# Performance work log

Hardware: AMD Instinct MI355X
Metric: run time of the kernel (lower is better)

Reference implementation:

```python
import jax, jax.numpy as jnp
import numpy as np

B, T, D = 4, 2048, 1024
H = 16
HD = D // H          # per-head dim (dk/heads = dv/heads = 64)
FF = 2048            # FFN default hidden_dim
EPS = 1e-5


def _ln(x, g, b):
    mu = jnp.mean(x, -1, keepdims=True)
    var = jnp.mean((x - mu) ** 2, -1, keepdims=True)
    return (x - mu) * jax.lax.rsqrt(var + EPS) * g + b


def setup_inputs() -> dict:
    key = jax.random.key(0)
    ks = jax.random.split(key, 12)
    s_in = 1.0 / np.sqrt(D)
    s_ff = 1.0 / np.sqrt(FF)
    return {
        "x": jax.random.normal(ks[0], (B, T, D), jnp.float32),
        # per-head projections stacked: [H, D, HD]
        "Wq": jax.random.uniform(ks[1], (H, D, HD), jnp.float32, -s_in, s_in),
        "bq": jnp.zeros((H, HD), jnp.float32),
        "Wk": jax.random.uniform(ks[2], (H, D, HD), jnp.float32, -s_in, s_in),
        "bk": jnp.zeros((H, HD), jnp.float32),
        "Wv": jax.random.uniform(ks[3], (H, D, HD), jnp.float32, -s_in, s_in),
        "bv": jnp.zeros((H, HD), jnp.float32),
        "Wo": jax.random.uniform(ks[4], (D, D), jnp.float32, -s_in, s_in),
        "bo": jnp.zeros((D,), jnp.float32),
        "ln1_g": jnp.ones((D,), jnp.float32),
        "ln1_b": jnp.zeros((D,), jnp.float32),
        "W1": jax.random.uniform(ks[5], (D, FF), jnp.float32, -s_in, s_in),
        "b1": jnp.zeros((FF,), jnp.float32),
        "W2": jax.random.uniform(ks[6], (FF, D), jnp.float32, -s_ff, s_ff),
        "b2": jnp.zeros((D,), jnp.float32),
        "ln2_g": jnp.ones((D,), jnp.float32),
        "ln2_b": jnp.zeros((D,), jnp.float32),
    }


def reference(x, Wq, bq, Wk, bk, Wv, bv, Wo, bo, ln1_g, ln1_b, W1, b1, W2, b2, ln2_g, ln2_b):
    # QKV projections (per-head Linear loop vectorized over H): [B,H,T,HD]
    q = jnp.einsum("btd,hdk->bhtk", x, Wq) + bq[:, None, :]
    k = jnp.einsum("btd,hdk->bhtk", x, Wk) + bk[:, None, :]
    v = jnp.einsum("btd,hdk->bhtk", x, Wv) + bv[:, None, :]
    # scaled dot-product attention; scale uses per-head dk = HD
    scores = jnp.einsum("bhtk,bhsk->bhts", q, k) / jnp.sqrt(jnp.float32(HD))
    weights = jax.nn.softmax(scores, axis=-1)
    ctx = jnp.einsum("bhts,bhsk->bhtk", weights, v)        # [B,H,T,HD]
    # concat heads along last dim (head order preserved) then output proj
    ctx = ctx.transpose(0, 2, 1, 3).reshape(B, T, D)
    c = ctx @ Wo + bo
    # residual + LayerNorm
    x = _ln(x + c, ln1_g, ln1_b)
    # FFN: Linear -> ReLU -> Linear
    y = jax.nn.relu(x @ W1 + b1) @ W2 + b2
    return _ln(x + y, ln2_g, ln2_b)
```

## Files before the change

### kernel.cpp

```cpp
#include <hip/hip_runtime.h>
#include <hip/hip_bf16.h>

#define BB 4
#define TT 2048
#define DD 1024
#define HH 16
#define HD 64
#define FF 2048
#define QSCL 0.1803368801111204f

typedef unsigned short u16;
typedef __bf16 bf16x8 __attribute__((ext_vector_type(8)));
typedef float f32x4 __attribute__((ext_vector_type(4)));
typedef float f32x16 __attribute__((ext_vector_type(16)));
typedef unsigned short u16x8 __attribute__((ext_vector_type(8)));
typedef unsigned short u16x4 __attribute__((ext_vector_type(4)));
typedef unsigned int u32x4 __attribute__((ext_vector_type(4)));

__device__ __forceinline__ u16 f2bf(float f) {
    return __builtin_bit_cast(u16, (__bf16)f);
}
__device__ __forceinline__ float bf2f(u16 u) {
    return __builtin_bit_cast(float, (unsigned)u << 16);
}
__device__ __forceinline__ float exp2fast(float x) {
    float r;
    asm("v_exp_f32 %0, %1" : "=v"(r) : "v"(x));
    return r;
}
__device__ __forceinline__ void gload16(const void* g, void* l) {
    __builtin_amdgcn_global_load_lds((const __attribute__((address_space(1))) void*)g,
                                     (__attribute__((address_space(3))) void*)l, 16, 0, 0);
}

__global__ __launch_bounds__(256) void convert_x(const float* __restrict__ in, u16* __restrict__ out, int n8) {
    int i = blockIdx.x * 256 + threadIdx.x;
    if (i >= n8) return;
    const float4* p = (const float4*)in + (size_t)i * 2;
    float4 a = p[0], b = p[1];
    u16x8 o;
    o[0] = f2bf(a.x); o[1] = f2bf(a.y); o[2] = f2bf(a.z); o[3] = f2bf(a.w);
    o[4] = f2bf(b.x); o[5] = f2bf(b.y); o[6] = f2bf(b.z); o[7] = f2bf(b.w);
    ((u16x8*)out)[i] = o;
}

__global__ __launch_bounds__(256) void transpose_conv(const float* __restrict__ in, u16* __restrict__ out, int R, int C) {
    __shared__ float tile[32][33];
    const int c0 = blockIdx.x * 32, r0 = blockIdx.y * 32;
    const int tx = threadIdx.x & 31, ty = threadIdx.x >> 5;
#pragma unroll
    for (int j = 0; j < 4; ++j) tile[ty + j * 8][tx] = in[(size_t)(r0 + ty + j * 8) * C + c0 + tx];
    __syncthreads();
#pragma unroll
    for (int j = 0; j < 4; ++j) out[(size_t)(c0 + ty + j * 8) * R + r0 + tx] = f2bf(tile[tx][ty + j * 8]);
}

__global__ __launch_bounds__(256) void qkv_transpose(const float* __restrict__ Wq, const float* __restrict__ Wk,
                                                     const float* __restrict__ Wv, u16* __restrict__ out) {
    __shared__ float tile[32][33];
    const int z = blockIdx.z, w = z >> 4, h = z & 15;
    const float* in = (w == 0 ? Wq : (w == 1 ? Wk : Wv)) + (size_t)h * (DD * HD);
    u16* op = out + (size_t)(w * 1024 + h * 64) * DD;
    const int c0 = blockIdx.x * 32, r0 = blockIdx.y * 32;
    const int tx = threadIdx.x & 31, ty = threadIdx.x >> 5;
#pragma unroll
    for (int j = 0; j < 4; ++j) tile[ty + j * 8][tx] = in[(size_t)(r0 + ty + j * 8) * HD + c0 + tx];
    __syncthreads();
#pragma unroll
    for (int j = 0; j < 4; ++j) op[(size_t)(c0 + ty + j * 8) * DD + r0 + tx] = f2bf(tile[tx][ty + j * 8]);
}

__global__ __launch_bounds__(256) void pack_bias(const float* __restrict__ bq, const float* __restrict__ bk,
                                                 const float* __restrict__ bv, float* __restrict__ out) {
    int i = blockIdx.x * 256 + threadIdx.x;
    if (i < 3072) {
        const float* s = i < 1024 ? bq : (i < 2048 ? bk : bv);
        out[i] = s[i & 1023];
    }
}

#define GBM 128
#define GBN 128
#define GBK 64

template <int EPI>
__global__ __launch_bounds__(256) void gemm_bt(const u16* __restrict__ A, const u16* __restrict__ Bt,
                                               const float* __restrict__ bias, const void* __restrict__ res,
                                               void* __restrict__ outp, void* __restrict__ outp2,
                                               int M, int N, int K) {
    __shared__ __align__(16) u16 sA[GBM * GBK];
    __shared__ __align__(16) u16 sB[GBN * GBK];
    const int t = threadIdx.x;
    const int lane = t & 63, wv = t >> 6;
    const int wm = (wv >> 1) * 64, wn = (wv & 1) * 64;
    const int lq = lane & 15, lk8 = (lane >> 4) * 8;
    const int nwg = gridDim.x * gridDim.y;
    const int bid = blockIdx.y * gridDim.x + blockIdx.x;
    const int swz = (bid & 7) * (nwg >> 3) + (bid >> 3);
    const int m0 = (swz / gridDim.x) * GBM, n0 = (swz % gridDim.x) * GBN;

    const int lr = lane >> 3, ch = lane & 7;
    const int colel = (ch ^ lr) << 3;
    const u16* Abase = A + (size_t)(m0 + wv * 32 + lr) * K + colel;
    const u16* Bbase = Bt + (size_t)(n0 + wv * 32 + lr) * K + colel;
    char* sAw = (char*)sA + wv * 32 * 128;
    char* sBw = (char*)sB + wv * 32 * 128;

    f32x4 acc[4][4];
#pragma unroll
    for (int i = 0; i < 4; ++i)
#pragma unroll
        for (int j = 0; j < 4; ++j) acc[i][j] = (f32x4){0.f, 0.f, 0.f, 0.f};

    for (int k0 = 0; k0 < K; k0 += GBK) {
#pragma unroll
        for (int i = 0; i < 4; ++i) {
            gload16(Abase + (size_t)i * 8 * K + k0, sAw + i * 1024);
            gload16(Bbase + (size_t)i * 8 * K + k0, sBw + i * 1024);
        }
        __syncthreads();
#pragma unroll
        for (int kk = 0; kk < 2; ++kk) {
            bf16x8 af[4], bfr[4];
#pragma unroll
            for (int mf = 0; mf < 4; ++mf) {
                int row = wm + mf * 16 + lq;
                int by = (row * 128 + kk * 64 + lk8 * 2) ^ ((row & 7) << 4);
                af[mf] = *(const bf16x8*)((const char*)sA + by);
            }
#pragma unroll
            for (int nf = 0; nf < 4; ++nf) {
                int row = wn + nf * 16 + lq;
                int by = (row * 128 + kk * 64 + lk8 * 2) ^ ((row & 7) << 4);
                bfr[nf] = *(const bf16x8*)((const char*)sB + by);
            }
#pragma unroll
            for (int mf = 0; mf < 4; ++mf)
#pragma unroll
                for (int nf = 0; nf < 4; ++nf)
                    acc[mf][nf] = __builtin_amdgcn_mfma_f32_16x16x32_bf16(af[mf], bfr[nf], acc[mf][nf], 0, 0, 0);
        }
        __syncthreads();
    }

    const int rbase = (lane >> 4) * 4;
#pragma unroll
    for (int mf = 0; mf < 4; ++mf) {
#pragma unroll
        for (int nf = 0; nf < 4; ++nf) {
            int gn = n0 + wn + nf * 16 + lq;
            float bv = bias[gn];
#pragma unroll
            for (int r = 0; r < 4; ++r) {
                int gm = m0 + wm + mf * 16 + rbase + r;
                size_t idx = (size_t)gm * N + gn;
                float val = acc[mf][nf][r] + bv;
                if (EPI == 2) {
                    ((u16*)outp)[idx] = f2bf(val > 0.f ? val : 0.f);
                } else if (EPI == 1) {
                    ((u16*)outp)[idx] = f2bf(val + ((const float*)res)[idx]);
                } else {
                    ((u16*)outp)[idx] = f2bf(val + bf2f(((const u16*)res)[idx]));
                }
            }
        }
    }
}

template <int EPI>
__global__ __launch_bounds__(512, 2) void gemm256(const u16* __restrict__ A, const u16* __restrict__ Bt,
                                                  const float* __restrict__ bias,
                                                  void* __restrict__ outp, void* __restrict__ outp2,
                                                  int M, int N, int K) {
    __shared__ __align__(16) u16 sA[2][256 * 64];
    __shared__ __align__(16) u16 sB[2][256 * 64];
    const int t = threadIdx.x;
    const int lane = t & 63, wv = t >> 6;
    const int wm = (wv >> 2) * 128, wn = (wv & 3) * 64;
    const int lq = lane & 15, lk8 = (lane >> 4) * 8;
    const int lr = lane >> 3, ch = lane & 7;
    const int colel = (ch ^ lr) << 3;
    const int nwg = gridDim.x * gridDim.y;
    const int bid = blockIdx.y * gridDim.x + blockIdx.x;
    const int swz = (bid & 7) * (nwg >> 3) + (bid >> 3);
    const int m0 = (swz / gridDim.x) * 256, n0 = (swz % gridDim.x) * 256;

    const u16* Ag = A + ((size_t)m0 + lr) * K + colel;
    const u16* Bg = Bt + ((size_t)n0 + lr) * K + colel;

#define STAGE_A(buf, slot, k0)                                                        \
    do {                                                                              \
        _Pragma("unroll") for (int j = 0; j < 2; ++j) {                               \
            int row0 = (slot)*64 + j * 128 + wv * 8;                                  \
            gload16(Ag + (size_t)row0 * K + (k0), (char*)sA + (buf)*32768 + row0 * 128); \
        }                                                                             \
    } while (0)
#define STAGE_B(buf, slot, k0)                                                        \
    do {                                                                              \
        _Pragma("unroll") for (int j = 0; j < 2; ++j) {                               \
            int c = j * 8 + wv;                                                       \
            int row0 = (c >> 2) * 64 + (slot)*32 + (c & 3) * 8;                       \
            gload16(Bg + (size_t)row0 * K + (k0), (char*)sB + (buf)*32768 + row0 * 128); \
        }                                                                             \
    } while (0)

    f32x4 acc[8][4];
#pragma unroll
    for (int i = 0; i < 8; ++i)
#pragma unroll
        for (int j = 0; j < 4; ++j) acc[i][j] = (f32x4){0.f, 0.f, 0.f, 0.f};

    STAGE_A(0, 0, 0);
    STAGE_B(0, 0, 0);
    STAGE_B(0, 1, 0);
    STAGE_A(0, 1, 0);
    asm volatile("s_waitcnt vmcnt(0)" ::: "memory");
    __builtin_amdgcn_s_barrier();
    __builtin_amdgcn_sched_barrier(0);

    const int nk = K / 64;
    for (int kt = 0; kt < nk; ++kt) {
        const int cur = kt & 1, nxt = cur ^ 1;
        const int k1 = (kt + 1) * 64;
        const bool pf = (kt + 1 < nk);
        const char* sAc = (const char*)sA + cur * 32768;
        const char* sBc = (const char*)sB + cur * 32768;
        bf16x8 a[4][2], b[4][2];

#pragma unroll
        for (int mf = 0; mf < 4; ++mf)
#pragma unroll
            for (int kk = 0; kk < 2; ++kk) {
                int row = wm + mf * 16 + lq;
                a[mf][kk] = *(const bf16x8*)(sAc + ((row * 128 + kk * 64 + lk8 * 2) ^ ((row & 7) << 4)));
            }
#pragma unroll
        for (int nf = 0; nf < 4; ++nf)
#pragma unroll
            for (int kk = 0; kk < 2; ++kk) {
                int row = wn + nf * 16 + lq;
                b[nf][kk] = *(const bf16x8*)(sBc + ((row * 128 + kk * 64 + lk8 * 2) ^ ((row & 7) << 4)));
            }
        if (pf) {
            STAGE_A(nxt, 0, k1);
            STAGE_B(nxt, 0, k1);
            STAGE_B(nxt, 1, k1);
        }
        asm volatile("s_waitcnt lgkmcnt(0)" ::: "memory");
        __builtin_amdgcn_sched_barrier(0);
        __builtin_amdgcn_s_setprio(1);
#pragma unroll
        for (int mf = 0; mf < 4; ++mf)
#pragma unroll
            for (int nf = 0; nf < 4; ++nf) {
                acc[mf][nf] = __builtin_amdgcn_mfma_f32_16x16x32_bf16(a[mf][0], b[nf][0], acc[mf][nf], 0, 0, 0);
                acc[mf][nf] = __builtin_amdgcn_mfma_f32_16x16x32_bf16(a[mf][1], b[nf][1], acc[mf][nf], 0, 0, 0);
            }
        __builtin_amdgcn_s_setprio(0);
        __builtin_amdgcn_sched_barrier(0);
        if (pf)
            asm volatile("s_waitcnt vmcnt(6)" ::: "memory");
        else
            asm volatile("s_waitcnt vmcnt(0)" ::: "memory");
        __builtin_amdgcn_s_barrier();
        __builtin_amdgcn_sched_barrier(0);

#pragma unroll
        for (int mf = 0; mf < 4; ++mf)
#pragma unroll
            for (int kk = 0; kk < 2; ++kk) {
                int row = wm + 64 + mf * 16 + lq;
                a[mf][kk] = *(const bf16x8*)(sAc + ((row * 128 + kk * 64 + lk8 * 2) ^ ((row & 7) << 4)));
            }
        if (pf) STAGE_A(nxt, 1, k1);
        asm volatile("s_waitcnt lgkmcnt(0)" ::: "memory");
        __builtin_amdgcn_sched_barrier(0);
        __builtin_amdgcn_s_setprio(1);
#pragma unroll
        for (int mf = 0; mf < 4; ++mf)
#pragma unroll
            for (int nf = 0; nf < 4; ++nf) {
                acc[mf + 4][nf] = __builtin_amdgcn_mfma_f32_16x16x32_bf16(a[mf][0], b[nf][0], acc[mf + 4][nf], 0, 0, 0);
                acc[mf + 4][nf] = __builtin_amdgcn_mfma_f32_16x16x32_bf16(a[mf][1], b[nf][1], acc[mf + 4][nf], 0, 0, 0);
            }
        __builtin_amdgcn_s_setprio(0);
        __builtin_amdgcn_sched_barrier(0);
        if (pf)
            asm volatile("s_waitcnt vmcnt(2)" ::: "memory");
        __builtin_amdgcn_s_barrier();
        __builtin_amdgcn_sched_barrier(0);
    }

    const int rbase = (lane >> 4) * 4;
#pragma unroll
    for (int mf = 0; mf < 8; ++mf) {
#pragma unroll
        for (int nf = 0; nf < 4; ++nf) {
            int gn = n0 + wn + nf * 16 + lq;
            float bv = bias[gn];
            if (EPI == 0) {
                int which = gn >> 10, hh = (gn >> 6) & 15, hd = gn & 63;
                int gm0 = m0 + wm + mf * 16 + rbase;
                int b2 = gm0 >> 11, tt2 = gm0 & 2047;
                if (which == 2) {
                    u16x4 pk;
#pragma unroll
                    for (int r = 0; r < 4; ++r) pk[r] = f2bf(acc[mf][nf][r] + bv);
                    *(u16x4*)((u16*)outp2 + ((size_t)(b2 * HH + hh) * HD + hd) * TT + tt2) = pk;
                } else {
                    float scl = (which == 0) ? QSCL : 1.f;
                    size_t off0 = (size_t)which * ((size_t)BB * HH * TT * HD) +
                                  ((size_t)(b2 * HH + hh) * TT + tt2) * HD + hd;
#pragma unroll
                    for (int r = 0; r < 4; ++r)
                        ((u16*)outp)[off0 + (size_t)r * HD] = f2bf((acc[mf][nf][r] + bv) * scl);
                }
            } else {
#pragma unroll
                for (int r = 0; r < 4; ++r) {
                    int gm = m0 + wm + mf * 16 + rbase + r;
                    float val = acc[mf][nf][r] + bv;
                    ((u16*)outp)[(size_t)gm * N + gn] = f2bf(val > 0.f ? val : 0.f);
                }
            }
        }
    }
#undef STAGE_A
#undef STAGE_B
}

__global__ __launch_bounds__(512) void attn_kernel(const u16* __restrict__ qk, const u16* __restrict__ vt,
                                                   u16* __restrict__ ctx) {
    const int t = threadIdx.x, wv = t >> 6, lane = t & 63;
    const int l31 = lane & 31, hi = lane >> 5;
    const int lr = lane >> 3, ch = lane & 7;
    const int colel = (ch ^ lr) << 3;
    const int bid = blockIdx.y * 8 + blockIdx.x;
    const int swz = (bid & 7) * 64 + (bid >> 3);
    const int qt = swz & 7, bh = swz >> 3;
    const size_t WSTR = (size_t)BB * HH * TT * HD;
    const u16* qp = qk + (size_t)bh * TT * HD;
    const u16* kp = qp + WSTR;
    const u16* vtp = vt + (size_t)bh * HD * TT;
    const int qr = qt * 256 + wv * 32;

    __shared__ __align__(16) u16 sK[2][64 * 64];
    __shared__ __align__(16) u16 sVt[2][64 * 64];

    const u16* kbase = kp + (size_t)(wv * 8 + lr) * HD + colel;
    const u16* vbase = vtp + (size_t)(wv * 8 + lr) * TT + colel;
    char* dK = (char*)sK + wv * 1024;
    char* dV = (char*)sVt + wv * 1024;

#define ATTN_STAGE(bufi, kb)                                        \
    do {                                                            \
        gload16(kbase + (size_t)(kb)*HD, dK + (bufi)*8192);         \
        gload16(vbase + (kb), dV + (bufi)*8192);                    \
    } while (0)

    bf16x8 qf[4];
#pragma unroll
    for (int c = 0; c < 4; ++c)
        qf[c] = *(const bf16x8*)(qp + (size_t)(qr + l31) * HD + c * 16 + 8 * hi);

    int off[2][4];
#pragma unroll
    for (int half = 0; half < 2; ++half)
#pragma unroll
        for (int c = 0; c < 4; ++c) {
            int row = half * 32 + l31;
            off[half][c] = row * 128 + (((c * 16 + 8 * hi) * 2) ^ ((row & 7) << 4));
        }

    f32x16 psv = (f32x16)0.f;
    f32x16 oacc[2];
    oacc[0] = (f32x16)0.f;
    oacc[1] = (f32x16)0.f;

    ATTN_STAGE(0, 0);

    const int NT = TT / 64;
    for (int kt = 0; kt < NT; ++kt) {
        const int cur = kt & 1;
        if (kt + 1 < NT) {
            ATTN_STAGE(cur ^ 1, (kt + 1) * 64);
            asm volatile("s_waitcnt vmcnt(2)" ::: "memory");
        } else {
            asm volatile("s_waitcnt vmcnt(0)" ::: "memory");
        }
        __builtin_amdgcn_s_barrier();
        __builtin_amdgcn_sched_barrier(0);

        const char* sKc = (const char*)sK + cur * 8192;
        const char* sVc = (const char*)sVt + cur * 8192;

        f32x16 sacc[2];
        sacc[0] = (f32x16)0.f;
        sacc[1] = (f32x16)0.f;
#pragma unroll
        for (int kb2 = 0; kb2 < 2; ++kb2)
#pragma unroll
            for (int c = 0; c < 4; ++c) {
                bf16x8 kf = *(const bf16x8*)(sKc + off[kb2][c]);
                sacc[kb2] = __builtin_amdgcn_mfma_f32_32x32x16_bf16(kf, qf[c], sacc[kb2], 0, 0, 0);
            }

#pragma unroll
        for (int kb2 = 0; kb2 < 2; ++kb2) {
#pragma unroll
            for (int i = 0; i < 16; ++i) sacc[kb2][i] = exp2fast(sacc[kb2][i]);
            psv += sacc[kb2];
        }

        bf16x8 pfrag[4];
#pragma unroll
        for (int kb2 = 0; kb2 < 2; ++kb2)
#pragma unroll
            for (int c2 = 0; c2 < 2; ++c2) {
                const int base = c2 * 8;
                unsigned a0, a1, b0, b1;
                asm("v_cvt_pk_bf16_f32 %0, %1, %2" : "=v"(a0) : "v"(sacc[kb2][base + 0]), "v"(sacc[kb2][base + 1]));
                asm("v_cvt_pk_bf16_f32 %0, %1, %2" : "=v"(a1) : "v"(sacc[kb2][base + 2]), "v"(sacc[kb2][base + 3]));
                asm("v_cvt_pk_bf16_f32 %0, %1, %2" : "=v"(b0) : "v"(sacc[kb2][base + 4]), "v"(sacc[kb2][base + 5]));
                asm("v_cvt_pk_bf16_f32 %0, %1, %2" : "=v"(b1) : "v"(sacc[kb2][base + 6]), "v"(sacc[kb2][base + 7]));
                asm("v_permlane32_swap_b32 %0, %1" : "+v"(a0), "+v"(b0));
                asm("v_permlane32_swap_b32 %0, %1" : "+v"(a1), "+v"(b1));
                u32x4 w = {a0, a1, b0, b1};
                pfrag[kb2 * 2 + c2] = __builtin_bit_cast(bf16x8, w);
            }

#pragma unroll
        for (int db = 0; db < 2; ++db)
#pragma unroll
            for (int kc = 0; kc < 4; ++kc) {
                bf16x8 vf = *(const bf16x8*)(sVc + off[db][kc]);
                oacc[db] = __builtin_amdgcn_mfma_f32_32x32x16_bf16(vf, pfrag[kc], oacc[db], 0, 0, 0);
            }

        __builtin_amdgcn_sched_barrier(0);
        __builtin_amdgcn_s_barrier();
    }

    float ls = 0.f;
#pragma unroll
    for (int i = 0; i < 16; ++i) ls += psv[i];
    ls += __shfl_xor(ls, 32);
    const float inv = 1.f / ls;

    const int b = bh >> 4, h = bh & 15;
    u16* orow = ctx + ((size_t)b * TT + (qr + l31)) * DD + h * HD;
#pragma unroll
    for (int db = 0; db < 2; ++db)
#pragma unroll
        for (int rq = 0; rq < 4; ++rq) {
            u16x4 ov;
#pragma unroll
            for (int j = 0; j < 4; ++j) ov[j] = f2bf(oacc[db][rq * 4 + j] * inv);
            *(u16x4*)(orow + db * 32 + rq * 8 + 4 * hi) = ov;
        }
#undef ATTN_STAGE
}

template <bool OUTF32>
__global__ __launch_bounds__(256) void ln_kernel(const u16* __restrict__ y, const float* __restrict__ g,
                                                 const float* __restrict__ b, float* __restrict__ of,
                                                 u16* __restrict__ ob) {
    const int row = blockIdx.x, t = threadIdx.x;
    const u16x4 raw = *(const u16x4*)(y + (size_t)row * DD + t * 4);
    float v0 = bf2f(raw[0]), v1 = bf2f(raw[1]), v2 = bf2f(raw[2]), v3 = bf2f(raw[3]);
    float s = v0 + v1 + v2 + v3;
    float q = v0 * v0 + v1 * v1 + v2 * v2 + v3 * v3;
#pragma unroll
    for (int m = 1; m < 64; m <<= 1) {
        s += __shfl_xor(s, m);
        q += __shfl_xor(q, m);
    }
    __shared__ float red[8];
    const int wv = t >> 6, ln = t & 63;
    if (ln == 0) {
        red[wv] = s;
        red[4 + wv] = q;
    }
    __syncthreads();
    s = red[0] + red[1] + red[2] + red[3];
    q = red[4] + red[5] + red[6] + red[7];
    const float mu = s * (1.f / DD);
    const float var = q * (1.f / DD) - mu * mu;
    const float rstd = rsqrtf(var + 1e-5f);
    const float4 gg = ((const float4*)g)[t];
    const float4 bb = ((const float4*)b)[t];
    float o0 = (v0 - mu) * rstd * gg.x + bb.x;
    float o1 = (v1 - mu) * rstd * gg.y + bb.y;
    float o2 = (v2 - mu) * rstd * gg.z + bb.z;
    float o3 = (v3 - mu) * rstd * gg.w + bb.w;
    if (OUTF32) {
        ((float4*)(of + (size_t)row * DD))[t] = (float4){o0, o1, o2, o3};
    } else {
        u16x4 u;
        u[0] = f2bf(o0); u[1] = f2bf(o1); u[2] = f2bf(o2); u[3] = f2bf(o3);
        *(u16x4*)(ob + (size_t)row * DD + t * 4) = u;
    }
}

extern "C" void kernel_launch(void* const* d_in, const int* in_sizes, int n_in,
                              void* d_out, int out_size, void* d_ws, size_t ws_size,
                              hipStream_t stream) {
    const float* x   = (const float*)d_in[0];
    const float* Wq  = (const float*)d_in[1];
    const float* bq  = (const float*)d_in[2];
    const float* Wk  = (const float*)d_in[3];
    const float* bk  = (const float*)d_in[4];
    const float* Wv  = (const float*)d_in[5];
    const float* bv  = (const float*)d_in[6];
    const float* Wo  = (const float*)d_in[7];
    const float* bo  = (const float*)d_in[8];
    const float* g1  = (const float*)d_in[9];
    const float* be1 = (const float*)d_in[10];
    const float* W1  = (const float*)d_in[11];
    const float* b1  = (const float*)d_in[12];
    const float* W2  = (const float*)d_in[13];
    const float* b2  = (const float*)d_in[14];
    const float* g2  = (const float*)d_in[15];
    const float* be2 = (const float*)d_in[16];
    float* out = (float*)d_out;

    char* ws = (char*)d_ws;
    u16*   xb    = (u16*)(ws + 0);
    u16*   wqkvt = (u16*)(ws + 16777216);
    u16*   wot   = (u16*)(ws + 23068672);
    u16*   w1t   = (u16*)(ws + 25165824);
    u16*   w2t   = (u16*)(ws + 29360128);
    float* bqkv  = (float*)(ws + 33554432);
    u16*   qkb   = (u16*)(ws + 33566720);
    u16*   vtb   = qkb + (size_t)2 * BB * HH * TT * HD;
    u16*   y1b   = (u16*)(ws + 83898368);
    u16*   x1b   = (u16*)(ws + 100675584);
    u16*   ctx   = xb;
    u16*   hbuf  = qkb;
    u16*   y2b   = y1b;

    const int M = BB * TT;

    convert_x<<<dim3((M * DD / 8 + 255) / 256), 256, 0, stream>>>(x, xb, M * DD / 8);
    qkv_transpose<<<dim3(2, 32, 48), 256, 0, stream>>>(Wq, Wk, Wv, wqkvt);
    transpose_conv<<<dim3(32, 32), 256, 0, stream>>>(Wo, wot, DD, DD);
    transpose_conv<<<dim3(64, 32), 256, 0, stream>>>(W1, w1t, DD, FF);
    transpose_conv<<<dim3(32, 64), 256, 0, stream>>>(W2, w2t, FF, DD);
    pack_bias<<<dim3(12), 256, 0, stream>>>(bq, bk, bv, bqkv);

    gemm256<0><<<dim3(3 * DD / 256, M / 256), 512, 0, stream>>>(xb, wqkvt, bqkv, qkb, vtb, M, 3 * DD, DD);
    attn_kernel<<<dim3(TT / 256, BB * HH), 512, 0, stream>>>(qkb, vtb, ctx);
    gemm_bt<1><<<dim3(DD / GBN, M / GBM), 256, 0, stream>>>(ctx, wot, bo, x, y1b, nullptr, M, DD, DD);
    ln_kernel<false><<<dim3(M), 256, 0, stream>>>(y1b, g1, be1, nullptr, x1b);
    gemm256<2><<<dim3(FF / 256, M / 256), 512, 0, stream>>>(x1b, w1t, b1, hbuf, nullptr, M, FF, DD);
    gemm_bt<3><<<dim3(DD / GBN, M / GBM), 256, 0, stream>>>(hbuf, w2t, b2, x1b, y2b, nullptr, M, DD, FF);
    ln_kernel<true><<<dim3(M), 256, 0, stream>>>(y2b, g2, be2, out, nullptr);
}
```

Before: 289.7 us.

## Process 64 query rows per wave in attention with 256-thread blocks

```diff
diff --git a/kernel.cpp b/kernel.cpp
--- a/kernel.cpp
+++ b/kernel.cpp
@@ -329,7 +329,7 @@
 #undef STAGE_B
 }
 
-__global__ __launch_bounds__(512) void attn_kernel(const u16* __restrict__ qk, const u16* __restrict__ vt,
+__global__ __launch_bounds__(256) void attn_kernel(const u16* __restrict__ qk, const u16* __restrict__ vt,
                                                    u16* __restrict__ ctx) {
     const int t = threadIdx.x, wv = t >> 6, lane = t & 63;
     const int l31 = lane & 31, hi = lane >> 5;
@@ -342,26 +342,30 @@
     const u16* qp = qk + (size_t)bh * TT * HD;
     const u16* kp = qp + WSTR;
     const u16* vtp = vt + (size_t)bh * HD * TT;
-    const int qr = qt * 256 + wv * 32;
+    const int qr = qt * 256 + wv * 64;
 
     __shared__ __align__(16) u16 sK[2][64 * 64];
     __shared__ __align__(16) u16 sVt[2][64 * 64];
 
-    const u16* kbase = kp + (size_t)(wv * 8 + lr) * HD + colel;
-    const u16* vbase = vtp + (size_t)(wv * 8 + lr) * TT + colel;
-    char* dK = (char*)sK + wv * 1024;
-    char* dV = (char*)sVt + wv * 1024;
-
-#define ATTN_STAGE(bufi, kb)                                        \
-    do {                                                            \
-        gload16(kbase + (size_t)(kb)*HD, dK + (bufi)*8192);         \
-        gload16(vbase + (kb), dV + (bufi)*8192);                    \
+    const u16* kbase = kp + (size_t)(wv * 16 + lr) * HD + colel;
+    const u16* vbase = vtp + (size_t)(wv * 16 + lr) * TT + colel;
+    char* dK = (char*)sK + wv * 16 * 128;
+    char* dV = (char*)sVt + wv * 16 * 128;
+
+#define ATTN_STAGE(bufi, kb)                                                              \
+    do {                                                                                  \
+        _Pragma("unroll") for (int ii = 0; ii < 2; ++ii) {                                \
+            gload16(kbase + (size_t)((kb) + ii * 8) * HD, dK + (bufi)*8192 + ii * 1024);  \
+            gload16(vbase + (size_t)(ii * 8) * TT + (kb), dV + (bufi)*8192 + ii * 1024);  \
+        }                                                                                 \
     } while (0)
 
-    bf16x8 qf[4];
-#pragma unroll
-    for (int c = 0; c < 4; ++c)
-        qf[c] = *(const bf16x8*)(qp + (size_t)(qr + l31) * HD + c * 16 + 8 * hi);
+    bf16x8 qf[2][4];
+#pragma unroll
+    for (int qg = 0; qg < 2; ++qg)
+#pragma unroll
+        for (int c = 0; c < 4; ++c)
+            qf[qg][c] = *(const bf16x8*)(qp + (size_t)(qr + qg * 32 + l31) * HD + c * 16 + 8 * hi);
 
     int off[2][4];
 #pragma unroll
@@ -372,10 +376,13 @@
             off[half][c] = row * 128 + (((c * 16 + 8 * hi) * 2) ^ ((row & 7) << 4));
         }
 
-    f32x16 psv = (f32x16)0.f;
-    f32x16 oacc[2];
-    oacc[0] = (f32x16)0.f;
-    oacc[1] = (f32x16)0.f;
+    float ls[2] = {0.f, 0.f};
+    f32x16 oacc[2][2];
+#pragma unroll
+    for (int qg = 0; qg < 2; ++qg) {
+        oacc[qg][0] = (f32x16)0.f;
+        oacc[qg][1] = (f32x16)0.f;
+    }
 
     ATTN_STAGE(0, 0);
 
@@ -384,7 +391,7 @@
         const int cur = kt & 1;
         if (kt + 1 < NT) {
             ATTN_STAGE(cur ^ 1, (kt + 1) * 64);
-            asm volatile("s_waitcnt vmcnt(2)" ::: "memory");
+            asm volatile("s_waitcnt vmcnt(4)" ::: "memory");
         } else {
             asm volatile("s_waitcnt vmcnt(0)" ::: "memory");
         }
@@ -394,70 +401,78 @@
         const char* sKc = (const char*)sK + cur * 8192;
         const char* sVc = (const char*)sVt + cur * 8192;
 
-        f32x16 sacc[2];
-        sacc[0] = (f32x16)0.f;
-        sacc[1] = (f32x16)0.f;
+        f32x16 sacc[2][2];
+#pragma unroll
+        for (int qg = 0; qg < 2; ++qg) {
+            sacc[qg][0] = (f32x16)0.f;
+            sacc[qg][1] = (f32x16)0.f;
+        }
 #pragma unroll
         for (int kb2 = 0; kb2 < 2; ++kb2)
 #pragma unroll
             for (int c = 0; c < 4; ++c) {
                 bf16x8 kf = *(const bf16x8*)(sKc + off[kb2][c]);
-                sacc[kb2] = __builtin_amdgcn_mfma_f32_32x32x16_bf16(kf, qf[c], sacc[kb2], 0, 0, 0);
-            }
-
-#pragma unroll
-        for (int kb2 = 0; kb2 < 2; ++kb2) {
-#pragma unroll
-            for (int i = 0; i < 16; ++i) sacc[kb2][i] = exp2fast(sacc[kb2][i]);
-            psv += sacc[kb2];
-        }
-
-        bf16x8 pfrag[4];
-#pragma unroll
-        for (int kb2 = 0; kb2 < 2; ++kb2)
-#pragma unroll
-            for (int c2 = 0; c2 < 2; ++c2) {
-                const int base = c2 * 8;
-                unsigned a0, a1, b0, b1;
-                asm("v_cvt_pk_bf16_f32 %0, %1, %2" : "=v"(a0) : "v"(sacc[kb2][base + 0]), "v"(sacc[kb2][base + 1]));
-                asm("v_cvt_pk_bf16_f32 %0, %1, %2" : "=v"(a1) : "v"(sacc[kb2][base + 2]), "v"(sacc[kb2][base + 3]));
-                asm("v_cvt_pk_bf16_f32 %0, %1, %2" : "=v"(b0) : "v"(sacc[kb2][base + 4]), "v"(sacc[kb2][base + 5]));
-                asm("v_cvt_pk_bf16_f32 %0, %1, %2" : "=v"(b1) : "v"(sacc[kb2][base + 6]), "v"(sacc[kb2][base + 7]));
-                asm("v_permlane32_swap_b32 %0, %1" : "+v"(a0), "+v"(b0));
-                asm("v_permlane32_swap_b32 %0, %1" : "+v"(a1), "+v"(b1));
-                u32x4 w = {a0, a1, b0, b1};
-                pfrag[kb2 * 2 + c2] = __builtin_bit_cast(bf16x8, w);
-            }
+                sacc[0][kb2] = __builtin_amdgcn_mfma_f32_32x32x16_bf16(kf, qf[0][c], sacc[0][kb2], 0, 0, 0);
+                sacc[1][kb2] = __builtin_amdgcn_mfma_f32_32x32x16_bf16(kf, qf[1][c], sacc[1][kb2], 0, 0, 0);
+            }
+
+        bf16x8 pfrag[2][4];
+#pragma unroll
+        for (int qg = 0; qg < 2; ++qg) {
+#pragma unroll
+            for (int kb2 = 0; kb2 < 2; ++kb2)
+#pragma unroll
+                for (int i = 0; i < 16; ++i) sacc[qg][kb2][i] = exp2fast(sacc[qg][kb2][i]);
+            f32x16 sm = sacc[qg][0] + sacc[qg][1];
+            float s8 = ((sm[0] + sm[1]) + (sm[2] + sm[3])) + ((sm[4] + sm[5]) + (sm[6] + sm[7]));
+            float s16 = ((sm[8] + sm[9]) + (sm[10] + sm[11])) + ((sm[12] + sm[13]) + (sm[14] + sm[15]));
+            ls[qg] += s8 + s16;
+#pragma unroll
+            for (int kb2 = 0; kb2 < 2; ++kb2)
+#pragma unroll
+                for (int c2 = 0; c2 < 2; ++c2) {
+                    const int base = c2 * 8;
+                    unsigned a0, a1, b0, b1;
+                    asm("v_cvt_pk_bf16_f32 %0, %1, %2" : "=v"(a0) : "v"(sacc[qg][kb2][base + 0]), "v"(sacc[qg][kb2][base + 1]));
+                    asm("v_cvt_pk_bf16_f32 %0, %1, %2" : "=v"(a1) : "v"(sacc[qg][kb2][base + 2]), "v"(sacc[qg][kb2][base + 3]));
+                    asm("v_cvt_pk_bf16_f32 %0, %1, %2" : "=v"(b0) : "v"(sacc[qg][kb2][base + 4]), "v"(sacc[qg][kb2][base + 5]));
+                    asm("v_cvt_pk_bf16_f32 %0, %1, %2" : "=v"(b1) : "v"(sacc[qg][kb2][base + 6]), "v"(sacc[qg][kb2][base + 7]));
+                    asm("v_permlane32_swap_b32 %0, %1" : "+v"(a0), "+v"(b0));
+                    asm("v_permlane32_swap_b32 %0, %1" : "+v"(a1), "+v"(b1));
+                    u32x4 w = {a0, a1, b0, b1};
+                    pfrag[qg][kb2 * 2 + c2] = __builtin_bit_cast(bf16x8, w);
+                }
+        }
 
 #pragma unroll
         for (int db = 0; db < 2; ++db)
 #pragma unroll
             for (int kc = 0; kc < 4; ++kc) {
                 bf16x8 vf = *(const bf16x8*)(sVc + off[db][kc]);
-                oacc[db] = __builtin_amdgcn_mfma_f32_32x32x16_bf16(vf, pfrag[kc], oacc[db], 0, 0, 0);
+                oacc[0][db] = __builtin_amdgcn_mfma_f32_32x32x16_bf16(vf, pfrag[0][kc], oacc[0][db], 0, 0, 0);
+                oacc[1][db] = __builtin_amdgcn_mfma_f32_32x32x16_bf16(vf, pfrag[1][kc], oacc[1][db], 0, 0, 0);
             }
 
         __builtin_amdgcn_sched_barrier(0);
         __builtin_amdgcn_s_barrier();
     }
 
-    float ls = 0.f;
-#pragma unroll
-    for (int i = 0; i < 16; ++i) ls += psv[i];
-    ls += __shfl_xor(ls, 32);
-    const float inv = 1.f / ls;
-
     const int b = bh >> 4, h = bh & 15;
-    u16* orow = ctx + ((size_t)b * TT + (qr + l31)) * DD + h * HD;
-#pragma unroll
-    for (int db = 0; db < 2; ++db)
-#pragma unroll
-        for (int rq = 0; rq < 4; ++rq) {
-            u16x4 ov;
-#pragma unroll
-            for (int j = 0; j < 4; ++j) ov[j] = f2bf(oacc[db][rq * 4 + j] * inv);
-            *(u16x4*)(orow + db * 32 + rq * 8 + 4 * hi) = ov;
-        }
+#pragma unroll
+    for (int qg = 0; qg < 2; ++qg) {
+        float l2 = ls[qg] + __shfl_xor(ls[qg], 32);
+        const float inv = 1.f / l2;
+        u16* orow = ctx + ((size_t)b * TT + (qr + qg * 32 + l31)) * DD + h * HD;
+#pragma unroll
+        for (int db = 0; db < 2; ++db)
+#pragma unroll
+            for (int rq = 0; rq < 4; ++rq) {
+                u16x4 ov;
+#pragma unroll
+                for (int j = 0; j < 4; ++j) ov[j] = f2bf(oacc[qg][db][rq * 4 + j] * inv);
+                *(u16x4*)(orow + db * 32 + rq * 8 + 4 * hi) = ov;
+            }
+    }
 #undef ATTN_STAGE
 }
 
@@ -549,7 +564,7 @@
     pack_bias<<<dim3(12), 256, 0, stream>>>(bq, bk, bv, bqkv);
 
     gemm256<0><<<dim3(3 * DD / 256, M / 256), 512, 0, stream>>>(xb, wqkvt, bqkv, qkb, vtb, M, 3 * DD, DD);
-    attn_kernel<<<dim3(TT / 256, BB * HH), 512, 0, stream>>>(qkb, vtb, ctx);
+    attn_kernel<<<dim3(8, BB * HH), 256, 0, stream>>>(qkb, vtb, ctx);
     gemm_bt<1><<<dim3(DD / GBN, M / GBM), 256, 0, stream>>>(ctx, wot, bo, x, y1b, nullptr, M, DD, DD);
     ln_kernel<false><<<dim3(M), 256, 0, stream>>>(y1b, g1, be1, nullptr, x1b);
     gemm256<2><<<dim3(FF / 256, M / 256), 512, 0, stream>>>(x1b, w1t, b1, hbuf, nullptr, M, FF, DD);
```

Result: slower. 324.5 us (+12.0%).

## Route Wo and W2 GEMMs through double-buffered gemm256 with 256x128 tiles

Applied to the files above, without the earlier changes.

```diff
diff --git a/kernel.cpp b/kernel.cpp
--- a/kernel.cpp
+++ b/kernel.cpp
@@ -79,140 +79,52 @@
     }
 }
 
-#define GBM 128
-#define GBN 128
-#define GBK 64
-
-template <int EPI>
-__global__ __launch_bounds__(256) void gemm_bt(const u16* __restrict__ A, const u16* __restrict__ Bt,
-                                               const float* __restrict__ bias, const void* __restrict__ res,
-                                               void* __restrict__ outp, void* __restrict__ outp2,
-                                               int M, int N, int K) {
-    __shared__ __align__(16) u16 sA[GBM * GBK];
-    __shared__ __align__(16) u16 sB[GBN * GBK];
+template <int EPI, int BN>
+__global__ __launch_bounds__(512, 2) void gemm256(const u16* __restrict__ A, const u16* __restrict__ Bt,
+                                                  const float* __restrict__ bias, const void* __restrict__ res,
+                                                  void* __restrict__ outp, void* __restrict__ outp2,
+                                                  int M, int N, int K) {
+    constexpr int NFR = BN / 64;
+    constexpr int NB = BN / 64;
+    __shared__ __align__(16) u16 sA[2][256 * 64];
+    __shared__ __align__(16) u16 sB[2][BN * 64];
     const int t = threadIdx.x;
     const int lane = t & 63, wv = t >> 6;
-    const int wm = (wv >> 1) * 64, wn = (wv & 1) * 64;
-    const int lq = lane & 15, lk8 = (lane >> 4) * 8;
-    const int nwg = gridDim.x * gridDim.y;
-    const int bid = blockIdx.y * gridDim.x + blockIdx.x;
-    const int swz = (bid & 7) * (nwg >> 3) + (bid >> 3);
-    const int m0 = (swz / gridDim.x) * GBM, n0 = (swz % gridDim.x) * GBN;
-
-    const int lr = lane >> 3, ch = lane & 7;
-    const int colel = (ch ^ lr) << 3;
-    const u16* Abase = A + (size_t)(m0 + wv * 32 + lr) * K + colel;
-    const u16* Bbase = Bt + (size_t)(n0 + wv * 32 + lr) * K + colel;
-    char* sAw = (char*)sA + wv * 32 * 128;
-    char* sBw = (char*)sB + wv * 32 * 128;
-
-    f32x4 acc[4][4];
-#pragma unroll
-    for (int i = 0; i < 4; ++i)
-#pragma unroll
-        for (int j = 0; j < 4; ++j) acc[i][j] = (f32x4){0.f, 0.f, 0.f, 0.f};
-
-    for (int k0 = 0; k0 < K; k0 += GBK) {
-#pragma unroll
-        for (int i = 0; i < 4; ++i) {
-            gload16(Abase + (size_t)i * 8 * K + k0, sAw + i * 1024);
-            gload16(Bbase + (size_t)i * 8 * K + k0, sBw + i * 1024);
-        }
-        __syncthreads();
-#pragma unroll
-        for (int kk = 0; kk < 2; ++kk) {
-            bf16x8 af[4], bfr[4];
-#pragma unroll
-            for (int mf = 0; mf < 4; ++mf) {
-                int row = wm + mf * 16 + lq;
-                int by = (row * 128 + kk * 64 + lk8 * 2) ^ ((row & 7) << 4);
-                af[mf] = *(const bf16x8*)((const char*)sA + by);
-            }
-#pragma unroll
-            for (int nf = 0; nf < 4; ++nf) {
-                int row = wn + nf * 16 + lq;
-                int by = (row * 128 + kk * 64 + lk8 * 2) ^ ((row & 7) << 4);
-                bfr[nf] = *(const bf16x8*)((const char*)sB + by);
-            }
-#pragma unroll
-            for (int mf = 0; mf < 4; ++mf)
-#pragma unroll
-                for (int nf = 0; nf < 4; ++nf)
-                    acc[mf][nf] = __builtin_amdgcn_mfma_f32_16x16x32_bf16(af[mf], bfr[nf], acc[mf][nf], 0, 0, 0);
-        }
-        __syncthreads();
-    }
-
-    const int rbase = (lane >> 4) * 4;
-#pragma unroll
-    for (int mf = 0; mf < 4; ++mf) {
-#pragma unroll
-        for (int nf = 0; nf < 4; ++nf) {
-            int gn = n0 + wn + nf * 16 + lq;
-            float bv = bias[gn];
-#pragma unroll
-            for (int r = 0; r < 4; ++r) {
-                int gm = m0 + wm + mf * 16 + rbase + r;
-                size_t idx = (size_t)gm * N + gn;
-                float val = acc[mf][nf][r] + bv;
-                if (EPI == 2) {
-                    ((u16*)outp)[idx] = f2bf(val > 0.f ? val : 0.f);
-                } else if (EPI == 1) {
-                    ((u16*)outp)[idx] = f2bf(val + ((const float*)res)[idx]);
-                } else {
-                    ((u16*)outp)[idx] = f2bf(val + bf2f(((const u16*)res)[idx]));
-                }
-            }
-        }
-    }
-}
-
-template <int EPI>
-__global__ __launch_bounds__(512, 2) void gemm256(const u16* __restrict__ A, const u16* __restrict__ Bt,
-                                                  const float* __restrict__ bias,
-                                                  void* __restrict__ outp, void* __restrict__ outp2,
-                                                  int M, int N, int K) {
-    __shared__ __align__(16) u16 sA[2][256 * 64];
-    __shared__ __align__(16) u16 sB[2][256 * 64];
-    const int t = threadIdx.x;
-    const int lane = t & 63, wv = t >> 6;
-    const int wm = (wv >> 2) * 128, wn = (wv & 3) * 64;
+    const int wm = (wv >> 2) * 128, wn = (wv & 3) * (BN / 4);
     const int lq = lane & 15, lk8 = (lane >> 4) * 8;
     const int lr = lane >> 3, ch = lane & 7;
     const int colel = (ch ^ lr) << 3;
     const int nwg = gridDim.x * gridDim.y;
     const int bid = blockIdx.y * gridDim.x + blockIdx.x;
     const int swz = (bid & 7) * (nwg >> 3) + (bid >> 3);
-    const int m0 = (swz / gridDim.x) * 256, n0 = (swz % gridDim.x) * 256;
+    const int m0 = (swz / gridDim.x) * 256, n0 = (swz % gridDim.x) * BN;
 
     const u16* Ag = A + ((size_t)m0 + lr) * K + colel;
     const u16* Bg = Bt + ((size_t)n0 + lr) * K + colel;
 
-#define STAGE_A(buf, slot, k0)                                                        \
-    do {                                                                              \
-        _Pragma("unroll") for (int j = 0; j < 2; ++j) {                               \
-            int row0 = (slot)*64 + j * 128 + wv * 8;                                  \
+#define STAGE_A(buf, slot, k0)                                                           \
+    do {                                                                                 \
+        _Pragma("unroll") for (int j = 0; j < 2; ++j) {                                  \
+            int row0 = (slot)*64 + j * 128 + wv * 8;                                     \
             gload16(Ag + (size_t)row0 * K + (k0), (char*)sA + (buf)*32768 + row0 * 128); \
-        }                                                                             \
+        }                                                                                \
     } while (0)
-#define STAGE_B(buf, slot, k0)                                                        \
-    do {                                                                              \
-        _Pragma("unroll") for (int j = 0; j < 2; ++j) {                               \
-            int c = j * 8 + wv;                                                       \
-            int row0 = (c >> 2) * 64 + (slot)*32 + (c & 3) * 8;                       \
-            gload16(Bg + (size_t)row0 * K + (k0), (char*)sB + (buf)*32768 + row0 * 128); \
-        }                                                                             \
+#define STAGE_B(buf, k0)                                                                          \
+    do {                                                                                          \
+        _Pragma("unroll") for (int j = 0; j < NB; ++j) {                                          \
+            int row0 = j * 64 + wv * 8;                                                           \
+            gload16(Bg + (size_t)row0 * K + (k0), (char*)sB + (buf) * (BN * 128) + row0 * 128);   \
+        }                                                                                         \
     } while (0)
 
-    f32x4 acc[8][4];
+    f32x4 acc[8][NFR];
 #pragma unroll
     for (int i = 0; i < 8; ++i)
 #pragma unroll
-        for (int j = 0; j < 4; ++j) acc[i][j] = (f32x4){0.f, 0.f, 0.f, 0.f};
+        for (int j = 0; j < NFR; ++j) acc[i][j] = (f32x4){0.f, 0.f, 0.f, 0.f};
 
     STAGE_A(0, 0, 0);
-    STAGE_B(0, 0, 0);
-    STAGE_B(0, 1, 0);
+    STAGE_B(0, 0);
     STAGE_A(0, 1, 0);
     asm volatile("s_waitcnt vmcnt(0)" ::: "memory");
     __builtin_amdgcn_s_barrier();
@@ -224,8 +136,8 @@
         const int k1 = (kt + 1) * 64;
         const bool pf = (kt + 1 < nk);
         const char* sAc = (const char*)sA + cur * 32768;
-        const char* sBc = (const char*)sB + cur * 32768;
-        bf16x8 a[4][2], b[4][2];
+        const char* sBc = (const char*)sB + cur * (BN * 128);
+        bf16x8 a[4][2], b[NFR][2];
 
 #pragma unroll
         for (int mf = 0; mf < 4; ++mf)
@@ -235,7 +147,7 @@
                 a[mf][kk] = *(const bf16x8*)(sAc + ((row * 128 + kk * 64 + lk8 * 2) ^ ((row & 7) << 4)));
             }
 #pragma unroll
-        for (int nf = 0; nf < 4; ++nf)
+        for (int nf = 0; nf < NFR; ++nf)
 #pragma unroll
             for (int kk = 0; kk < 2; ++kk) {
                 int row = wn + nf * 16 + lq;
@@ -243,8 +155,7 @@
             }
         if (pf) {
             STAGE_A(nxt, 0, k1);
-            STAGE_B(nxt, 0, k1);
-            STAGE_B(nxt, 1, k1);
+            STAGE_B(nxt, k1);
         }
         asm volatile("s_waitcnt lgkmcnt(0)" ::: "memory");
         __builtin_amdgcn_sched_barrier(0);
@@ -252,16 +163,20 @@
 #pragma unroll
         for (int mf = 0; mf < 4; ++mf)
 #pragma unroll
-            for (int nf = 0; nf < 4; ++nf) {
+            for (int nf = 0; nf < NFR; ++nf) {
                 acc[mf][nf] = __builtin_amdgcn_mfma_f32_16x16x32_bf16(a[mf][0], b[nf][0], acc[mf][nf], 0, 0, 0);
                 acc[mf][nf] = __builtin_amdgcn_mfma_f32_16x16x32_bf16(a[mf][1], b[nf][1], acc[mf][nf], 0, 0, 0);
             }
         __builtin_amdgcn_s_setprio(0);
         __builtin_amdgcn_sched_barrier(0);
-        if (pf)
-            asm volatile("s_waitcnt vmcnt(6)" ::: "memory");
-        else
+        if (pf) {
+            if (BN == 256)
+                asm volatile("s_waitcnt vmcnt(6)" ::: "memory");
+            else
+                asm volatile("s_waitcnt vmcnt(4)" ::: "memory");
+        } else {
             asm volatile("s_waitcnt vmcnt(0)" ::: "memory");
+        }
         __builtin_amdgcn_s_barrier();
         __builtin_amdgcn_sched_barrier(0);
 
@@ -279,7 +194,7 @@
 #pragma unroll
         for (int mf = 0; mf < 4; ++mf)
 #pragma unroll
-            for (int nf = 0; nf < 4; ++nf) {
+            for (int nf = 0; nf < NFR; ++nf) {
                 acc[mf + 4][nf] = __builtin_amdgcn_mfma_f32_16x16x32_bf16(a[mf][0], b[nf][0], acc[mf + 4][nf], 0, 0, 0);
                 acc[mf + 4][nf] = __builtin_amdgcn_mfma_f32_16x16x32_bf16(a[mf][1], b[nf][1], acc[mf + 4][nf], 0, 0, 0);
             }
@@ -295,7 +210,7 @@
 #pragma unroll
     for (int mf = 0; mf < 8; ++mf) {
 #pragma unroll
-        for (int nf = 0; nf < 4; ++nf) {
+        for (int nf = 0; nf < NFR; ++nf) {
             int gn = n0 + wn + nf * 16 + lq;
             float bv = bias[gn];
             if (EPI == 0) {
@@ -319,8 +234,15 @@
 #pragma unroll
                 for (int r = 0; r < 4; ++r) {
                     int gm = m0 + wm + mf * 16 + rbase + r;
+                    size_t idx = (size_t)gm * N + gn;
                     float val = acc[mf][nf][r] + bv;
-                    ((u16*)outp)[(size_t)gm * N + gn] = f2bf(val > 0.f ? val : 0.f);
+                    if (EPI == 2) {
+                        ((u16*)outp)[idx] = f2bf(val > 0.f ? val : 0.f);
+                    } else if (EPI == 1) {
+                        ((u16*)outp)[idx] = f2bf(val + ((const float*)res)[idx]);
+                    } else {
+                        ((u16*)outp)[idx] = f2bf(val + bf2f(((const u16*)res)[idx]));
+                    }
                 }
             }
         }
@@ -548,11 +470,11 @@
     transpose_conv<<<dim3(32, 64), 256, 0, stream>>>(W2, w2t, FF, DD);
     pack_bias<<<dim3(12), 256, 0, stream>>>(bq, bk, bv, bqkv);
 
-    gemm256<0><<<dim3(3 * DD / 256, M / 256), 512, 0, stream>>>(xb, wqkvt, bqkv, qkb, vtb, M, 3 * DD, DD);
-    attn_kernel<<<dim3(TT / 256, BB * HH), 512, 0, stream>>>(qkb, vtb, ctx);
-    gemm_bt<1><<<dim3(DD / GBN, M / GBM), 256, 0, stream>>>(ctx, wot, bo, x, y1b, nullptr, M, DD, DD);
+    gemm256<0, 256><<<dim3(3 * DD / 256, M / 256), 512, 0, stream>>>(xb, wqkvt, bqkv, nullptr, qkb, vtb, M, 3 * DD, DD);
+    attn_kernel<<<dim3(8, BB * HH), 512, 0, stream>>>(qkb, vtb, ctx);
+    gemm256<1, 128><<<dim3(DD / 128, M / 256), 512, 0, stream>>>(ctx, wot, bo, x, y1b, nullptr, M, DD, DD);
     ln_kernel<false><<<dim3(M), 256, 0, stream>>>(y1b, g1, be1, nullptr, x1b);
-    gemm256<2><<<dim3(FF / 256, M / 256), 512, 0, stream>>>(x1b, w1t, b1, hbuf, nullptr, M, FF, DD);
-    gemm_bt<3><<<dim3(DD / GBN, M / GBM), 256, 0, stream>>>(hbuf, w2t, b2, x1b, y2b, nullptr, M, DD, FF);
+    gemm256<2, 256><<<dim3(FF / 256, M / 256), 512, 0, stream>>>(x1b, w1t, b1, nullptr, hbuf, nullptr, M, FF, DD);
+    gemm256<3, 128><<<dim3(DD / 128, M / 256), 512, 0, stream>>>(hbuf, w2t, b2, x1b, y2b, nullptr, M, DD, FF);
     ln_kernel<true><<<dim3(M), 256, 0, stream>>>(y2b, g2, be2, out, nullptr);
 }
```

Result: no change. 285.0 us (-1.6%).
